# Optimization experiments

Hardware: AMD Instinct MI355X
Metric: run time of the kernel (lower is better)

## Reference

```python
import jax, jax.numpy as jnp
import numpy as np

NN_SIZE = 10  # k nearest neighbors (includes the point itself)
EPS = 1e-8


def batch_normals(points_nchw, nn_size):
    # points_nchw: (B, 3, N)
    x = jnp.transpose(points_nchw, (0, 2, 1))  # (B, N, 3)
    sq = jnp.sum(x * x, axis=-1)  # (B, N)
    # pairwise squared distances (B, N, N)
    d2 = sq[:, :, None] + sq[:, None, :] - 2.0 * jnp.einsum('bnd,bmd->bnm', x, x)
    _, idx = jax.lax.top_k(-d2, nn_size)  # (B, N, k) nearest-neighbor indices
    # irregular gather of neighborhoods: (B, N, k, 3)
    neigh = jax.vmap(lambda p, i: p[i])(x, idx)
    centered = neigh - jnp.mean(neigh, axis=2, keepdims=True)
    # local 3x3 covariance per point
    cov = jnp.einsum('bnki,bnkj->bnij', centered, centered) / nn_size
    _, vecs = jnp.linalg.eigh(cov)  # eigenvalues ascending
    normals = vecs[..., 0]  # eigenvector of smallest eigenvalue, (B, N, 3), unit norm
    return jnp.transpose(normals, (0, 2, 1))  # (B, 3, N)


def setup_inputs() -> dict:
    key = jax.random.key(0)
    k1, k2 = jax.random.split(key)
    pred = jax.random.normal(k1, (8, 3, 4096), dtype=jnp.float32)
    gt = jax.random.normal(k2, (8, 3, 4096), dtype=jnp.float32)
    return {"pred": pred, "gt": gt}


def reference(pred, gt):
    pn = batch_normals(pred, NN_SIZE)  # (B, 3, N)
    gn = batch_normals(gt, NN_SIZE)    # (B, 3, N)
    # cosine similarity along the channel (coordinate) dim
    dot = jnp.sum(pn * gn, axis=1)
    denom = jnp.sqrt(jnp.sum(pn * pn, axis=1)) * jnp.sqrt(jnp.sum(gn * gn, axis=1))
    cos = dot / jnp.maximum(denom, EPS)
    return jnp.mean(1.0 - jnp.abs(cos))
```

## Files before the change

kernel.cpp:

```cpp
#include <hip/hip_runtime.h>
#include <float.h>
#include <math.h>

#define BATCH 8
#define NPTS 4096
#define KNN 10
#define BN (BATCH * NPTS)
#define TPB 1024
#define WAVES 16
#define Q 4
#define QPB (64 * Q)
#define SEGC (NPTS / WAVES)
#define KB_STRIDE (Q * KNN + 1)

__device__ float4 g_nrm[2 * BN];

__device__ inline float med3f(float x, float a, float b) {
    return __builtin_amdgcn_fmed3f(x, a, b);
}

#define INSERT(karr, key)                                              \
    do {                                                               \
        _Pragma("unroll")                                              \
        for (int _j = KNN - 1; _j >= 1; --_j)                          \
            karr[_j] = med3f((key), karr[_j - 1], karr[_j]);           \
        karr[0] = fminf((key), karr[0]);                               \
    } while (0)

#define PROC(_p, _gi)                                                  \
    do {                                                               \
        float _d0 = fmaf((_p).z, a0z, fmaf((_p).y, a0y, fmaf((_p).x, a0x, (_p).w))); \
        float _d1 = fmaf((_p).z, a1z, fmaf((_p).y, a1y, fmaf((_p).x, a1x, (_p).w))); \
        float _d2 = fmaf((_p).z, a2z, fmaf((_p).y, a2y, fmaf((_p).x, a2x, (_p).w))); \
        float _d3 = fmaf((_p).z, a3z, fmaf((_p).y, a3y, fmaf((_p).x, a3x, (_p).w))); \
        float _k0 = __uint_as_float((__float_as_uint(_d0) & 0xFFFFF000u) | (_gi)); \
        float _k1 = __uint_as_float((__float_as_uint(_d1) & 0xFFFFF000u) | (_gi)); \
        float _k2 = __uint_as_float((__float_as_uint(_d2) & 0xFFFFF000u) | (_gi)); \
        float _k3 = __uint_as_float((__float_as_uint(_d3) & 0xFFFFF000u) | (_gi)); \
        INSERT(kq0, _k0);                                              \
        INSERT(kq1, _k1);                                              \
        INSERT(kq2, _k2);                                              \
        INSERT(kq3, _k3);                                              \
    } while (0)

#define PROC4(P, _gi)                                                  \
    do {                                                               \
        PROC(P##0, (_gi) + 0);                                         \
        PROC(P##1, (_gi) + 1);                                         \
        PROC(P##2, (_gi) + 2);                                         \
        PROC(P##3, (_gi) + 3);                                         \
    } while (0)

#define LOAD4(P, _off)                                                 \
    do {                                                               \
        P##0 = pts[(_off) + 0]; P##1 = pts[(_off) + 1];                \
        P##2 = pts[(_off) + 2]; P##3 = pts[(_off) + 3];                \
    } while (0)

__device__ inline void smallest_eigvec(float a00, float a01, float a02,
                                       float a11, float a12, float a22,
                                       float& vx, float& vy, float& vz) {
    float p1 = a01 * a01 + a02 * a02 + a12 * a12;
    float q = (a00 + a11 + a22) * (1.0f / 3.0f);
    float b00 = a00 - q, b11 = a11 - q, b22 = a22 - q;
    float p2 = b00 * b00 + b11 * b11 + b22 * b22 + 2.0f * p1;
    float p = sqrtf(p2 * (1.0f / 6.0f));
    if (p < 1e-20f) { vx = 1.0f; vy = 0.0f; vz = 0.0f; return; }
    float ip = 1.0f / p;
    float c00 = b00 * ip, c01 = a01 * ip, c02 = a02 * ip;
    float c11 = b11 * ip, c12 = a12 * ip, c22 = b22 * ip;
    float detB = c00 * (c11 * c22 - c12 * c12)
               - c01 * (c01 * c22 - c12 * c02)
               + c02 * (c01 * c12 - c11 * c02);
    float r = 0.5f * detB;
    r = fminf(1.0f, fmaxf(-1.0f, r));
    float phi = acosf(r) * (1.0f / 3.0f);
    float lmin = q + 2.0f * p * cosf(phi + 2.0943951023931953f);

    float m00 = a00 - lmin, m11 = a11 - lmin, m22 = a22 - lmin;
    float r0x = m00, r0y = a01, r0z = a02;
    float r1x = a01, r1y = m11, r1z = a12;
    float r2x = a02, r2y = a12, r2z = m22;
    float c0x = r0y * r1z - r0z * r1y, c0y = r0z * r1x - r0x * r1z, c0z = r0x * r1y - r0y * r1x;
    float c1x = r0y * r2z - r0z * r2y, c1y = r0z * r2x - r0x * r2z, c1z = r0x * r2y - r0y * r2x;
    float c2x = r1y * r2z - r1z * r2y, c2y = r1z * r2x - r1x * r2z, c2z = r1x * r2y - r1y * r2x;
    float n0 = c0x * c0x + c0y * c0y + c0z * c0z;
    float n1 = c1x * c1x + c1y * c1y + c1z * c1z;
    float n2 = c2x * c2x + c2y * c2y + c2z * c2z;
    float bx = c0x, by = c0y, bz = c0z, bnm = n0;
    if (n1 > bnm) { bx = c1x; by = c1y; bz = c1z; bnm = n1; }
    if (n2 > bnm) { bx = c2x; by = c2y; bz = c2z; bnm = n2; }
    if (bnm < 1e-30f) { vx = 1.0f; vy = 0.0f; vz = 0.0f; return; }
    float inv = rsqrtf(bnm);
    vx = bx * inv; vy = by * inv; vz = bz * inv;
}

__global__ void zero_out_kernel(float* __restrict__ out) {
    if (threadIdx.x == 0) out[0] = 0.0f;
}

__global__ __launch_bounds__(TPB, 4) void knn_normals(
    const float* __restrict__ pred, const float* __restrict__ gt) {
    __shared__ float4 pts[NPTS + 8];
    __shared__ float keybuf[8 * 64 * KB_STRIDE];

    const int b = blockIdx.y;
    const int cloud = blockIdx.z;
    const float* __restrict__ base = (cloud ? gt : pred) + b * 3 * NPTS;
    const int tid = threadIdx.x;
    const int lane = tid & 63;
    const int w = tid >> 6;
    const int s0 = w * SEGC;
    const int qbase = blockIdx.x * QPB;

    for (int i = tid; i < NPTS; i += TPB) {
        float x = base[i];
        float y = base[NPTS + i];
        float z = base[2 * NPTS + i];
        pts[i] = make_float4(x, y, z, fmaf(x, x, fmaf(y, y, z * z)));
    }
    __syncthreads();

    const int q0 = qbase + lane;
    const float a0x = -2.0f * pts[q0].x,       a0y = -2.0f * pts[q0].y,       a0z = -2.0f * pts[q0].z;
    const float a1x = -2.0f * pts[q0 + 64].x,  a1y = -2.0f * pts[q0 + 64].y,  a1z = -2.0f * pts[q0 + 64].z;
    const float a2x = -2.0f * pts[q0 + 128].x, a2y = -2.0f * pts[q0 + 128].y, a2z = -2.0f * pts[q0 + 128].z;
    const float a3x = -2.0f * pts[q0 + 192].x, a3y = -2.0f * pts[q0 + 192].y, a3z = -2.0f * pts[q0 + 192].z;

    float kq0[KNN], kq1[KNN], kq2[KNN], kq3[KNN];
#pragma unroll
    for (int j = 0; j < KNN; ++j) { kq0[j] = FLT_MAX; kq1[j] = FLT_MAX; kq2[j] = FLT_MAX; kq3[j] = FLT_MAX; }

    {
        const unsigned gb = (unsigned)s0;
        float4 A0, A1, A2, A3;
        float4 B0, B1, B2, B3;
        LOAD4(A, s0);
        __builtin_amdgcn_sched_barrier(0);
        for (int c = 0; c < SEGC; c += 8) {
            LOAD4(B, s0 + c + 4);
            __builtin_amdgcn_sched_barrier(0);
            PROC4(A, gb + (unsigned)c);
            __builtin_amdgcn_sched_barrier(0);
            LOAD4(A, s0 + c + 8);
            __builtin_amdgcn_sched_barrier(0);
            PROC4(B, gb + (unsigned)c + 4u);
            __builtin_amdgcn_sched_barrier(0);
        }
    }

    for (int half = WAVES / 2; half >= 1; half >>= 1) {
        if (w >= half && w < 2 * half) {
            float* dst = keybuf + ((w - half) * 64 + lane) * KB_STRIDE;
#pragma unroll
            for (int j = 0; j < KNN; ++j) {
                dst[j] = kq0[j];
                dst[KNN + j] = kq1[j];
                dst[2 * KNN + j] = kq2[j];
                dst[3 * KNN + j] = kq3[j];
            }
        }
        __syncthreads();
        if (w < half) {
            const float* src = keybuf + (w * 64 + lane) * KB_STRIDE;
#pragma unroll
            for (int j = 0; j < KNN; ++j) {
                float s0v = src[j], s1v = src[KNN + j], s2v = src[2 * KNN + j], s3v = src[3 * KNN + j];
                INSERT(kq0, s0v);
                INSERT(kq1, s1v);
                INSERT(kq2, s2v);
                INSERT(kq3, s3v);
            }
        }
        __syncthreads();
    }

    if (w == 0) {
        float* dst = keybuf + lane * KB_STRIDE;
#pragma unroll
        for (int j = 0; j < KNN; ++j) {
            dst[j] = kq0[j];
            dst[KNN + j] = kq1[j];
            dst[2 * KNN + j] = kq2[j];
            dst[3 * KNN + j] = kq3[j];
        }
    }
    __syncthreads();
    if (w < Q) {
        const float* src = keybuf + lane * KB_STRIDE + w * KNN;
        float sx = 0.f, sy = 0.f, sz = 0.f;
        float sxx = 0.f, sxy = 0.f, sxz = 0.f;
        float syy = 0.f, syz = 0.f, szz = 0.f;
#pragma unroll
        for (int j = 0; j < KNN; ++j) {
            int idx = (int)(__float_as_uint(src[j]) & 0xFFFu);
            float4 nb = pts[idx];
            sx += nb.x; sy += nb.y; sz += nb.z;
            sxx = fmaf(nb.x, nb.x, sxx); sxy = fmaf(nb.x, nb.y, sxy); sxz = fmaf(nb.x, nb.z, sxz);
            syy = fmaf(nb.y, nb.y, syy); syz = fmaf(nb.y, nb.z, syz); szz = fmaf(nb.z, nb.z, szz);
        }
        const float iK = 1.0f / KNN;
        float mx = sx * iK, my = sy * iK, mz = sz * iK;
        float vx, vy, vz;
        smallest_eigvec(sxx * iK - mx * mx, sxy * iK - mx * my,
                        sxz * iK - mx * mz, syy * iK - my * my,
                        syz * iK - my * mz, szz * iK - mz * mz,
                        vx, vy, vz);
        g_nrm[(cloud * BATCH + b) * NPTS + qbase + w * 64 + lane] = make_float4(vx, vy, vz, 0.f);
    }
}

__global__ __launch_bounds__(256) void cos_loss_kernel(float* __restrict__ out) {
    const int i = blockIdx.x * 256 + threadIdx.x;
    float4 p = g_nrm[i];
    float4 g = g_nrm[BN + i];
    float dot = p.x * g.x + p.y * g.y + p.z * g.z;
    float npn = sqrtf(p.x * p.x + p.y * p.y + p.z * p.z);
    float ngn = sqrtf(g.x * g.x + g.y * g.y + g.z * g.z);
    float acc = 1.0f - fabsf(dot / fmaxf(npn * ngn, 1e-8f));
    for (int off = 32; off > 0; off >>= 1) acc += __shfl_down(acc, off);
    if ((threadIdx.x & 63) == 0) atomicAdd(out, acc * (1.0f / (float)BN));
}

extern "C" void kernel_launch(void* const* d_in, const int* in_sizes, int n_in,
                              void* d_out, int out_size, void* d_ws, size_t ws_size,
                              hipStream_t stream) {
    const float* pred = (const float*)d_in[0];
    const float* gt = (const float*)d_in[1];
    float* out = (float*)d_out;

    zero_out_kernel<<<1, 64, 0, stream>>>(out);
    dim3 grid(NPTS / QPB, BATCH, 2);
    knn_normals<<<grid, TPB, 0, stream>>>(pred, gt);
    cos_loss_kernel<<<dim3(BN / 256), 256, 0, stream>>>(out);
}
```

Before: 172.6 us.

## Halve queries per thread, alias key buffer onto point LDS, raise occupancy

Each thread now tracks 2 query points instead of 4, which halves per-thread register state for the top-k lists and doubles the block count. The separate key-merge LDS buffer is dropped and aliased onto the point array, and an extra barrier is added before the merge. Because the point array is overwritten, the covariance stage now gathers neighbour coordinates from global memory. The aim is higher occupancy (launch bounds 8) and lower LDS use, at the cost of reloading the point cloud in twice as many blocks and doing scattered global gathers.

After: 173.0 us. About the same (+0.2%).

```diff
diff --git a/kernel.cpp b/kernel.cpp
--- a/kernel.cpp
+++ b/kernel.cpp
@@ -8,7 +8,7 @@
 #define BN (BATCH * NPTS)
 #define TPB 1024
 #define WAVES 16
-#define Q 4
+#define Q 2
 #define QPB (64 * Q)
 #define SEGC (NPTS / WAVES)
 #define KB_STRIDE (Q * KNN + 1)
@@ -31,30 +31,21 @@
     do {                                                               \
         float _d0 = fmaf((_p).z, a0z, fmaf((_p).y, a0y, fmaf((_p).x, a0x, (_p).w))); \
         float _d1 = fmaf((_p).z, a1z, fmaf((_p).y, a1y, fmaf((_p).x, a1x, (_p).w))); \
-        float _d2 = fmaf((_p).z, a2z, fmaf((_p).y, a2y, fmaf((_p).x, a2x, (_p).w))); \
-        float _d3 = fmaf((_p).z, a3z, fmaf((_p).y, a3y, fmaf((_p).x, a3x, (_p).w))); \
         float _k0 = __uint_as_float((__float_as_uint(_d0) & 0xFFFFF000u) | (_gi)); \
         float _k1 = __uint_as_float((__float_as_uint(_d1) & 0xFFFFF000u) | (_gi)); \
-        float _k2 = __uint_as_float((__float_as_uint(_d2) & 0xFFFFF000u) | (_gi)); \
-        float _k3 = __uint_as_float((__float_as_uint(_d3) & 0xFFFFF000u) | (_gi)); \
         INSERT(kq0, _k0);                                              \
         INSERT(kq1, _k1);                                              \
-        INSERT(kq2, _k2);                                              \
-        INSERT(kq3, _k3);                                              \
-    } while (0)
-
-#define PROC4(P, _gi)                                                  \
+    } while (0)
+
+#define PROC2(P, _gi)                                                  \
     do {                                                               \
         PROC(P##0, (_gi) + 0);                                         \
         PROC(P##1, (_gi) + 1);                                         \
-        PROC(P##2, (_gi) + 2);                                         \
-        PROC(P##3, (_gi) + 3);                                         \
-    } while (0)
-
-#define LOAD4(P, _off)                                                 \
+    } while (0)
+
+#define LOAD2(P, _off)                                                 \
     do {                                                               \
         P##0 = pts[(_off) + 0]; P##1 = pts[(_off) + 1];                \
-        P##2 = pts[(_off) + 2]; P##3 = pts[(_off) + 3];                \
     } while (0)
 
 __device__ inline void smallest_eigvec(float a00, float a01, float a02,
@@ -99,10 +90,10 @@
     if (threadIdx.x == 0) out[0] = 0.0f;
 }
 
-__global__ __launch_bounds__(TPB, 4) void knn_normals(
+__global__ __launch_bounds__(TPB, 8) void knn_normals(
     const float* __restrict__ pred, const float* __restrict__ gt) {
     __shared__ float4 pts[NPTS + 8];
-    __shared__ float keybuf[8 * 64 * KB_STRIDE];
+    float* keybuf = (float*)pts;
 
     const int b = blockIdx.y;
     const int cloud = blockIdx.z;
@@ -122,54 +113,45 @@
     __syncthreads();
 
     const int q0 = qbase + lane;
-    const float a0x = -2.0f * pts[q0].x,       a0y = -2.0f * pts[q0].y,       a0z = -2.0f * pts[q0].z;
-    const float a1x = -2.0f * pts[q0 + 64].x,  a1y = -2.0f * pts[q0 + 64].y,  a1z = -2.0f * pts[q0 + 64].z;
-    const float a2x = -2.0f * pts[q0 + 128].x, a2y = -2.0f * pts[q0 + 128].y, a2z = -2.0f * pts[q0 + 128].z;
-    const float a3x = -2.0f * pts[q0 + 192].x, a3y = -2.0f * pts[q0 + 192].y, a3z = -2.0f * pts[q0 + 192].z;
-
-    float kq0[KNN], kq1[KNN], kq2[KNN], kq3[KNN];
-#pragma unroll
-    for (int j = 0; j < KNN; ++j) { kq0[j] = FLT_MAX; kq1[j] = FLT_MAX; kq2[j] = FLT_MAX; kq3[j] = FLT_MAX; }
+    const float a0x = -2.0f * pts[q0].x,      a0y = -2.0f * pts[q0].y,      a0z = -2.0f * pts[q0].z;
+    const float a1x = -2.0f * pts[q0 + 64].x, a1y = -2.0f * pts[q0 + 64].y, a1z = -2.0f * pts[q0 + 64].z;
+
+    float kq0[KNN], kq1[KNN];
+#pragma unroll
+    for (int j = 0; j < KNN; ++j) { kq0[j] = FLT_MAX; kq1[j] = FLT_MAX; }
 
     {
         const unsigned gb = (unsigned)s0;
-        float4 A0, A1, A2, A3;
-        float4 B0, B1, B2, B3;
-        LOAD4(A, s0);
+        float4 A0, A1, B0, B1;
+        LOAD2(A, s0);
         __builtin_amdgcn_sched_barrier(0);
-        for (int c = 0; c < SEGC; c += 8) {
-            LOAD4(B, s0 + c + 4);
-            __builtin_amdgcn_sched_barrier(0);
-            PROC4(A, gb + (unsigned)c);
-            __builtin_amdgcn_sched_barrier(0);
-            LOAD4(A, s0 + c + 8);
-            __builtin_amdgcn_sched_barrier(0);
-            PROC4(B, gb + (unsigned)c + 4u);
-            __builtin_amdgcn_sched_barrier(0);
-        }
-    }
+        for (int c = 0; c < SEGC; c += 4) {
+            LOAD2(B, s0 + c + 2);
+            __builtin_amdgcn_sched_barrier(0);
+            PROC2(A, gb + (unsigned)c);
+            __builtin_amdgcn_sched_barrier(0);
+            LOAD2(A, s0 + c + 4);
+            __builtin_amdgcn_sched_barrier(0);
+            PROC2(B, gb + (unsigned)c + 2u);
+            __builtin_amdgcn_sched_barrier(0);
+        }
+    }
+    __syncthreads();
 
     for (int half = WAVES / 2; half >= 1; half >>= 1) {
         if (w >= half && w < 2 * half) {
             float* dst = keybuf + ((w - half) * 64 + lane) * KB_STRIDE;
 #pragma unroll
-            for (int j = 0; j < KNN; ++j) {
-                dst[j] = kq0[j];
-                dst[KNN + j] = kq1[j];
-                dst[2 * KNN + j] = kq2[j];
-                dst[3 * KNN + j] = kq3[j];
-            }
+            for (int j = 0; j < KNN; ++j) { dst[j] = kq0[j]; dst[KNN + j] = kq1[j]; }
         }
         __syncthreads();
         if (w < half) {
             const float* src = keybuf + (w * 64 + lane) * KB_STRIDE;
 #pragma unroll
             for (int j = 0; j < KNN; ++j) {
-                float s0v = src[j], s1v = src[KNN + j], s2v = src[2 * KNN + j], s3v = src[3 * KNN + j];
+                float s0v = src[j], s1v = src[KNN + j];
                 INSERT(kq0, s0v);
                 INSERT(kq1, s1v);
-                INSERT(kq2, s2v);
-                INSERT(kq3, s3v);
             }
         }
         __syncthreads();
@@ -178,12 +160,7 @@
     if (w == 0) {
         float* dst = keybuf + lane * KB_STRIDE;
 #pragma unroll
-        for (int j = 0; j < KNN; ++j) {
-            dst[j] = kq0[j];
-            dst[KNN + j] = kq1[j];
-            dst[2 * KNN + j] = kq2[j];
-            dst[3 * KNN + j] = kq3[j];
-        }
+        for (int j = 0; j < KNN; ++j) { dst[j] = kq0[j]; dst[KNN + j] = kq1[j]; }
     }
     __syncthreads();
     if (w < Q) {
@@ -194,10 +171,12 @@
 #pragma unroll
         for (int j = 0; j < KNN; ++j) {
             int idx = (int)(__float_as_uint(src[j]) & 0xFFFu);
-            float4 nb = pts[idx];
-            sx += nb.x; sy += nb.y; sz += nb.z;
-            sxx = fmaf(nb.x, nb.x, sxx); sxy = fmaf(nb.x, nb.y, sxy); sxz = fmaf(nb.x, nb.z, sxz);
-            syy = fmaf(nb.y, nb.y, syy); syz = fmaf(nb.y, nb.z, syz); szz = fmaf(nb.z, nb.z, szz);
+            float x = base[idx];
+            float y = base[NPTS + idx];
+            float z = base[2 * NPTS + idx];
+            sx += x; sy += y; sz += z;
+            sxx = fmaf(x, x, sxx); sxy = fmaf(x, y, sxy); sxz = fmaf(x, z, sxz);
+            syy = fmaf(y, y, syy); syz = fmaf(y, z, syz); szz = fmaf(z, z, szz);
         }
         const float iK = 1.0f / KNN;
         float mx = sx * iK, my = sy * iK, mz = sz * iK;
```
